# Kernel tuning notes

Measured on AMD Instinct MI355X. Metric: run time of the kernel, lower is better.

## Reference

```python
import jax, jax.numpy as jnp
import numpy as np
import math

NUM_HEADS = 3
WINDOW = 7


def _shift_masks(ws):
    # row_mask: block mask for windows wrapping across the bottom edge
    half = ws * (ws // 2)  # 21 for ws=7
    row = np.zeros((ws * ws, ws * ws), np.float32)
    row[-half:, :-half] = -np.inf
    row[:-half, -half:] = -np.inf
    # column_mask = rearrange(row, '(r w1) (c w2) -> (w1 r) (w2 c)')
    col = row.reshape(ws, ws, ws, ws).transpose(1, 0, 3, 2).reshape(ws * ws, ws * ws)
    return jnp.asarray(row), jnp.asarray(col)


def setup_inputs() -> dict:
    key = jax.random.key(0)
    ks = jax.random.split(key, 5)
    B, S, E = 64, 3136, 96
    return {
        'x': jax.random.normal(ks[0], (B, S, E), jnp.float32),
        'w1': jax.random.normal(ks[1], (3 * E, E), jnp.float32) * 0.05,
        'b1': jax.random.normal(ks[2], (3 * E,), jnp.float32) * 0.05,
        'w2': jax.random.normal(ks[3], (E, E), jnp.float32) * 0.05,
        'b2': jax.random.normal(ks[4], (E,), jnp.float32) * 0.05,
    }


def reference(x, w1, b1, w2, b2):
    b, S, E = x.shape
    h = w = int(math.sqrt(S))          # 56
    ws = WINDOW
    H = NUM_HEADS
    Eh = E // H                        # head dim = 32
    nh, nw = h // ws, w // ws          # windows per axis = 8
    scale = 1.0 / math.sqrt(E / H)
    # faithful to original: forward shift = -ws//2 = -4, inverse shift = ws//2 = 3
    shift_fwd = -ws // 2
    shift_bwd = ws // 2

    qkv = x @ w1.T + b1                              # [b, S, 3E]
    qkv = qkv.reshape(b, h, w, E, 3)                 # (c K) split, K fastest
    qkv = jnp.roll(qkv, (shift_fwd, shift_fwd), axis=(1, 2))
    # b (nh m1) (nw m2) (H Eh) K -> b H nh nw (m1 m2) Eh K
    qkv = qkv.reshape(b, nh, ws, nw, ws, H, Eh, 3)
    qkv = qkv.transpose(0, 5, 1, 3, 2, 4, 6, 7).reshape(b, H, nh, nw, ws * ws, Eh, 3)
    Q, K, V = qkv[..., 0], qkv[..., 1], qkv[..., 2]

    s = jnp.einsum('bHhwme,bHhwne->bHhwmn', Q, K) * scale  # [b,H,nh,nw,49,49]
    row_mask, col_mask = _shift_masks(ws)
    s = s.at[:, :, -1, :].add(row_mask)   # last row of windows
    s = s.at[:, :, :, -1].add(col_mask)   # last column of windows

    att = jax.nn.softmax(s, axis=-1)
    o = jnp.einsum('bHhwmn,bHhwne->bHhwme', att, V)        # [b,H,nh,nw,49,Eh]
    # b H nh nw (m1 m2) Eh -> b (nh m1) (nw m2) (H Eh)
    o = o.reshape(b, H, nh, nw, ws, ws, Eh)
    o = o.transpose(0, 2, 4, 3, 5, 1, 6).reshape(b, h, w, E)
    o = jnp.roll(o, (shift_bwd, shift_bwd), axis=(1, 2))
    o = o.reshape(b, S, E)
    return o @ w2.T + b2
```

## Files before the change

kernel.cpp:

```cpp
#include <hip/hip_runtime.h>


typedef _Float16 f16;
typedef _Float16 f16x4 __attribute__((ext_vector_type(4)));
typedef _Float16 f16x8 __attribute__((ext_vector_type(8)));
typedef float f32x4 __attribute__((ext_vector_type(4)));

static __device__ __forceinline__ f32x4 mfma16(f16x8 a, f16x8 b, f32x4 c) {
    return __builtin_amdgcn_mfma_f32_16x16x32_f16(a, b, c, 0, 0, 0);
}
static __device__ __forceinline__ f16x8 cvt8(const float* __restrict__ p) {
    float4 f0 = *(const float4*)(p);
    float4 f1 = *(const float4*)(p + 4);
    f16x8 h;
    h[0]=(f16)f0.x; h[1]=(f16)f0.y; h[2]=(f16)f0.z; h[3]=(f16)f0.w;
    h[4]=(f16)f1.x; h[5]=(f16)f1.y; h[6]=(f16)f1.z; h[7]=(f16)f1.w;
    return h;
}

#define SMEM_BYTES 38208
#define OFF_Q  7056
#define OFF_K  17248
#define OFF_VT 27440

template<bool WS>
__global__ __launch_bounds__(256, 4) void swin_fused(
    const float* __restrict__ x, const float* __restrict__ w1,
    const float* __restrict__ b1, const float* __restrict__ w2,
    const float* __restrict__ b2, float* __restrict__ out,
    const f16* __restrict__ w1p, const f16* __restrict__ w2p,
    const float* __restrict__ b1p)
{
    __shared__ __align__(16) char smem[SMEM_BYTES];
    f16* p_s  = (f16*)(smem);
    f16* q_s  = (f16*)(smem + OFF_Q);
    f16* k_s  = (f16*)(smem + OFF_K);
    f16* vt_s = (f16*)(smem + OFF_VT);
    f16* o_s  = q_s;

    const int tid  = threadIdx.x;
    const int wv   = tid >> 6;
    const int lane = tid & 63;
    const int lrow = lane & 15;
    const int lq   = lane >> 4;

    const int bx = blockIdx.x;
    const int b  = bx >> 6;
    const int wz = bx & 63;
    const int wh = wz >> 3;
    const int ww = wz & 7;

    const float* xb = x + b * (3136 * 96);

    if (tid < 96) {
        #pragma unroll
        for (int p7 = 49; p7 < 56; ++p7) vt_s[tid * 56 + p7] = (f16)0.f;
    }
    if (tid < 8) vt_s[96 * 56 + tid] = (f16)0.f;

    {
        f16x8 bf[5][3];
        float bias[5];
        int   kq[5], cm[5];
        #pragma unroll
        for (int t = 0; t < 5; ++t) {
            int nt = wv + 4 * t;
            if (nt < 18) {
                int col = nt * 16 + lrow;
                int kqv = nt / 6;
                int c96 = col - kqv * 96;
                if constexpr (WS) {
                    #pragma unroll
                    for (int ks = 0; ks < 3; ++ks)
                        bf[t][ks] = *(const f16x8*)(w1p + col * 96 + ks * 32 + lq * 8);
                    bias[t] = b1p[col];
                } else {
                    int srow = c96 * 3 + kqv;
                    #pragma unroll
                    for (int ks = 0; ks < 3; ++ks)
                        bf[t][ks] = cvt8(w1 + srow * 96 + ks * 32 + lq * 8);
                    bias[t] = b1[srow];
                }
                kq[t] = kqv; cm[t] = c96;
            } else { kq[t] = -1; cm[t] = 0; bias[t] = 0.f; }
        }
        #pragma unroll
        for (int mt = 0; mt < 4; ++mt) {
            int p  = mt * 16 + lrow; if (p > 48) p = 48;
            int i  = p / 7, j = p - i * 7;
            int r  = wh * 7 + i + 4; if (r >= 56) r -= 56;
            int c  = ww * 7 + j + 4; if (c >= 56) c -= 56;
            const float* xr = xb + (r * 56 + c) * 96;
            f16x8 af[3];
            #pragma unroll
            for (int ks = 0; ks < 3; ++ks) af[ks] = cvt8(xr + ks * 32 + lq * 8);
            int rbase = mt * 16 + lq * 4;
            #pragma unroll
            for (int t = 0; t < 5; ++t) {
                if (kq[t] < 0) continue;
                f32x4 acc = {0.f, 0.f, 0.f, 0.f};
                #pragma unroll
                for (int ks = 0; ks < 3; ++ks) acc = mfma16(af[ks], bf[t][ks], acc);
                if (kq[t] == 0) {
                    #pragma unroll
                    for (int r2 = 0; r2 < 4; ++r2) {
                        int row = rbase + r2;
                        if (row < 49) q_s[row * 104 + cm[t]] = (f16)(acc[r2] + bias[t]);
                    }
                } else if (kq[t] == 1) {
                    #pragma unroll
                    for (int r2 = 0; r2 < 4; ++r2) {
                        int row = rbase + r2;
                        if (row < 49) k_s[row * 104 + cm[t]] = (f16)(acc[r2] + bias[t]);
                    }
                } else {
                    f16x4 pk;
                    #pragma unroll
                    for (int r2 = 0; r2 < 4; ++r2) pk[r2] = (f16)(acc[r2] + bias[t]);
                    if (rbase < 45)      *(f16x4*)(vt_s + cm[t] * 56 + rbase) = pk;
                    else if (rbase == 48) vt_s[cm[t] * 56 + 48] = pk[0];
                }
            }
        }
    }
    __syncthreads();

    const bool mrow = (wh == 7), mcol = (ww == 7);
    const float scale = 0.17677669529663687f;
    const int mt = wv;
    const int arow  = mt * 16 + lrow;
    const int mbase = mt * 16 + lq * 4;

    #pragma unroll
    for (int hh = 0; hh < 3; ++hh) {
        f16x8 aq = *(const f16x8*)(q_s + arow * 104 + hh * 32 + lq * 8);
        f32x4 sc[4];
        #pragma unroll
        for (int nt = 0; nt < 4; ++nt) {
            f16x8 bk = *(const f16x8*)(k_s + (nt * 16 + lrow) * 104 + hh * 32 + lq * 8);
            f32x4 z = {0.f, 0.f, 0.f, 0.f};
            sc[nt] = mfma16(aq, bk, z);
        }
        float ev[4][4], vmax[4], esum[4];
        #pragma unroll
        for (int r2 = 0; r2 < 4; ++r2) vmax[r2] = -3e38f;
        #pragma unroll
        for (int nt = 0; nt < 4; ++nt) {
            int  nn  = nt * 16 + lrow;
            bool nok = nn < 49;
            bool nge = nn >= 28, n4 = (nn % 7) >= 4;
            #pragma unroll
            for (int r2 = 0; r2 < 4; ++r2) {
                int  mm = mbase + r2;
                bool ok = nok && (!mrow || ((mm >= 28) == nge))
                              && (!mcol || (((mm % 7) >= 4) == n4));
                float v = ok ? sc[nt][r2] * scale : -3e38f;
                ev[nt][r2] = v;
                vmax[r2] = fmaxf(vmax[r2], v);
            }
        }
        #pragma unroll
        for (int r2 = 0; r2 < 4; ++r2) {
            float m0 = vmax[r2];
            m0 = fmaxf(m0, __shfl_xor(m0, 1));
            m0 = fmaxf(m0, __shfl_xor(m0, 2));
            m0 = fmaxf(m0, __shfl_xor(m0, 4));
            m0 = fmaxf(m0, __shfl_xor(m0, 8));
            vmax[r2] = m0;
            esum[r2] = 0.f;
        }
        #pragma unroll
        for (int nt = 0; nt < 4; ++nt)
            #pragma unroll
            for (int r2 = 0; r2 < 4; ++r2) {
                float e = (ev[nt][r2] > -1e38f) ? __expf(ev[nt][r2] - vmax[r2]) : 0.f;
                ev[nt][r2] = e;
                esum[r2] += e;
            }
        #pragma unroll
        for (int r2 = 0; r2 < 4; ++r2) {
            float s = esum[r2];
            s += __shfl_xor(s, 1);
            s += __shfl_xor(s, 2);
            s += __shfl_xor(s, 4);
            s += __shfl_xor(s, 8);
            esum[r2] = 1.0f / s;
        }
        #pragma unroll
        for (int nt = 0; nt < 4; ++nt)
            #pragma unroll
            for (int r2 = 0; r2 < 4; ++r2) {
                int mm = mbase + r2;
                if (mm < 49)
                    p_s[mm * 72 + nt * 16 + lrow] = (f16)(ev[nt][r2] * esum[r2]);
            }

        f16x8 ap0 = *(const f16x8*)(p_s + arow * 72 + lq * 8);
        f16x8 ap1 = *(const f16x8*)(p_s + arow * 72 + 32 + lq * 8);
        #pragma unroll
        for (int et = 0; et < 2; ++et) {
            int vrow = hh * 32 + et * 16 + lrow;
            f16x8 bv0 = *(const f16x8*)(vt_s + vrow * 56 + lq * 8);
            f16x8 bv1 = *(const f16x8*)(vt_s + vrow * 56 + 32 + lq * 8);
            f32x4 z = {0.f, 0.f, 0.f, 0.f};
            f32x4 acc = mfma16(ap0, bv0, z);
            acc = mfma16(ap1, bv1, acc);
            #pragma unroll
            for (int r2 = 0; r2 < 4; ++r2) {
                int row = mbase + r2;
                if (row < 49)
                    o_s[row * 104 + hh * 32 + et * 16 + lrow] = (f16)acc[r2];
            }
        }
    }

    {
        f16x8 ao[3];
        #pragma unroll
        for (int ks = 0; ks < 3; ++ks)
            ao[ks] = *(const f16x8*)(o_s + arow * 104 + ks * 32 + lq * 8);
        int opos[4];
        #pragma unroll
        for (int r2 = 0; r2 < 4; ++r2) {
            int m  = mbase + r2;
            int mm = (m < 49) ? m : 48;
            int i  = mm / 7, j = mm - i * 7;
            int orow = wh * 7 + i + 3; if (orow >= 56) orow -= 56;
            int ocol = ww * 7 + j + 3; if (ocol >= 56) ocol -= 56;
            opos[r2] = (b * 3136 + orow * 56 + ocol) * 96;
        }
        #pragma unroll
        for (int nt = 0; nt < 6; ++nt) {
            int eo = nt * 16 + lrow;
            f32x4 acc = {0.f, 0.f, 0.f, 0.f};
            #pragma unroll
            for (int ks = 0; ks < 3; ++ks) {
                f16x8 hb;
                if constexpr (WS)
                    hb = *(const f16x8*)(w2p + eo * 96 + ks * 32 + lq * 8);
                else
                    hb = cvt8(w2 + eo * 96 + ks * 32 + lq * 8);
                acc = mfma16(ao[ks], hb, acc);
            }
            float bias = b2[eo];
            #pragma unroll
            for (int r2 = 0; r2 < 4; ++r2)
                if (mbase + r2 < 49) out[opos[r2] + eo] = acc[r2] + bias;
        }
    }
}

__global__ void prep_weights(const float* __restrict__ w1, const float* __restrict__ b1,
                             const float* __restrict__ w2,
                             f16* __restrict__ w1p, f16* __restrict__ w2p,
                             float* __restrict__ b1p)
{
    int idx = blockIdx.x * 256 + threadIdx.x;
    if (idx < 27648) {
        int np = idx / 96, k = idx - np * 96;
        int kq = np / 96, c96 = np - kq * 96;
        w1p[idx] = (f16)w1[(c96 * 3 + kq) * 96 + k];
    } else if (idx < 36864) {
        int i2 = idx - 27648;
        w2p[i2] = (f16)w2[i2];
    } else if (idx < 37152) {
        int np = idx - 36864;
        int kq = np / 96, c96 = np - kq * 96;
        b1p[np] = b1[c96 * 3 + kq];
    }
}

extern "C" void kernel_launch(void* const* d_in, const int* in_sizes, int n_in,
                              void* d_out, int out_size, void* d_ws, size_t ws_size,
                              hipStream_t stream) {
    const float* x  = (const float*)d_in[0];
    const float* w1 = (const float*)d_in[1];
    const float* b1 = (const float*)d_in[2];
    const float* w2 = (const float*)d_in[3];
    const float* b2 = (const float*)d_in[4];
    float* out = (float*)d_out;

    const size_t need = 27648u * 2 + 9216u * 2 + 288u * 4;
    if (ws_size >= need) {
        f16*   w1p = (f16*)d_ws;
        f16*   w2p = w1p + 27648;
        float* b1p = (float*)(w2p + 9216);
        prep_weights<<<dim3(146), dim3(256), 0, stream>>>(w1, b1, w2, w1p, w2p, b1p);
        swin_fused<true><<<dim3(4096), dim3(256), 0, stream>>>(
            x, w1, b1, w2, b2, out, w1p, w2p, b1p);
    } else {
        swin_fused<false><<<dim3(4096), dim3(256), 0, stream>>>(
            x, w1, b1, w2, b2, out, nullptr, nullptr, nullptr);
    }
}
```

Before: 226.5 us.

## Transpose MFMA operands so softmax stays in registers and stores vectorize

Swaps the A/B operands of the QKV, score, PV and output-projection MFMAs, so each lane owns one query row and the column results land contiguous per lane. The softmax reductions are then mostly in-register with two cross-lane shuffles, normalization is deferred to the PV output, and P is redistributed with register shuffles instead of being written to and read back from a shared-memory P buffer. This frees shared memory, allowing launch bounds to rise to 5 blocks per CU, and turns the Q/K, O and final output stores into 4-wide vector writes. The cost is extra shuffle instructions and more register pressure under the tighter occupancy bound.

New measurement: 258.9 us. 1.14x slower.

```diff
diff --git a/kernel.cpp b/kernel.cpp
--- a/kernel.cpp
+++ b/kernel.cpp
@@ -2,6 +2,7 @@
 
 
 typedef _Float16 f16;
+typedef _Float16 f16x2 __attribute__((ext_vector_type(2)));
 typedef _Float16 f16x4 __attribute__((ext_vector_type(4)));
 typedef _Float16 f16x8 __attribute__((ext_vector_type(8)));
 typedef float f32x4 __attribute__((ext_vector_type(4)));
@@ -18,13 +19,15 @@
     return h;
 }
 
-#define SMEM_BYTES 38208
-#define OFF_Q  7056
-#define OFF_K  17248
-#define OFF_VT 27440
+#define SMEM_BYTES 31152
+#define OFF_K  10192
+#define OFF_VT 20384
+
+union U2 { int i; f16x2 h; };
+union U8 { int i[4]; f16x8 h; };
 
 template<bool WS>
-__global__ __launch_bounds__(256, 4) void swin_fused(
+__global__ __launch_bounds__(256, 5) void swin_fused(
     const float* __restrict__ x, const float* __restrict__ w1,
     const float* __restrict__ b1, const float* __restrict__ w2,
     const float* __restrict__ b2, float* __restrict__ out,
@@ -32,8 +35,7 @@
     const float* __restrict__ b1p)
 {
     __shared__ __align__(16) char smem[SMEM_BYTES];
-    f16* p_s  = (f16*)(smem);
-    f16* q_s  = (f16*)(smem + OFF_Q);
+    f16* q_s  = (f16*)(smem);
     f16* k_s  = (f16*)(smem + OFF_K);
     f16* vt_s = (f16*)(smem + OFF_VT);
     f16* o_s  = q_s;
@@ -60,65 +62,74 @@
 
     {
         f16x8 bf[5][3];
-        float bias[5];
-        int   kq[5], cm[5];
+        int   kq[5], cb[5];
         #pragma unroll
         for (int t = 0; t < 5; ++t) {
-            int nt = wv + 4 * t;
-            if (nt < 18) {
-                int col = nt * 16 + lrow;
-                int kqv = nt / 6;
-                int c96 = col - kqv * 96;
+            int ot = wv + 4 * t;
+            if (ot < 18) {
+                int kqv = ot / 6;
+                kq[t] = kqv;
+                cb[t] = (ot - kqv * 6) * 16;
                 if constexpr (WS) {
                     #pragma unroll
                     for (int ks = 0; ks < 3; ++ks)
-                        bf[t][ks] = *(const f16x8*)(w1p + col * 96 + ks * 32 + lq * 8);
-                    bias[t] = b1p[col];
+                        bf[t][ks] = *(const f16x8*)(w1p + (ot*16 + lrow)*96 + ks*32 + lq*8);
                 } else {
-                    int srow = c96 * 3 + kqv;
+                    int srowA = (ot*16 + lrow - kqv*96) * 3 + kqv;
                     #pragma unroll
                     for (int ks = 0; ks < 3; ++ks)
-                        bf[t][ks] = cvt8(w1 + srow * 96 + ks * 32 + lq * 8);
-                    bias[t] = b1[srow];
+                        bf[t][ks] = cvt8(w1 + srowA*96 + ks*32 + lq*8);
                 }
-                kq[t] = kqv; cm[t] = c96;
-            } else { kq[t] = -1; cm[t] = 0; bias[t] = 0.f; }
-        }
-        #pragma unroll
-        for (int mt = 0; mt < 4; ++mt) {
-            int p  = mt * 16 + lrow; if (p > 48) p = 48;
-            int i  = p / 7, j = p - i * 7;
+            } else kq[t] = -1;
+        }
+        #pragma unroll
+        for (int pt = 0; pt < 4; ++pt) {
+            int p  = pt * 16 + lrow;
+            int pc = (p < 49) ? p : 48;
+            int i  = pc / 7, j = pc - i * 7;
             int r  = wh * 7 + i + 4; if (r >= 56) r -= 56;
             int c  = ww * 7 + j + 4; if (c >= 56) c -= 56;
             const float* xr = xb + (r * 56 + c) * 96;
-            f16x8 af[3];
-            #pragma unroll
-            for (int ks = 0; ks < 3; ++ks) af[ks] = cvt8(xr + ks * 32 + lq * 8);
-            int rbase = mt * 16 + lq * 4;
+            f16x8 xf[3];
+            #pragma unroll
+            for (int ks = 0; ks < 3; ++ks) xf[ks] = cvt8(xr + ks * 32 + lq * 8);
+            const bool pok = (p < 49);
             #pragma unroll
             for (int t = 0; t < 5; ++t) {
                 if (kq[t] < 0) continue;
+                int ot = wv + 4 * t;
                 f32x4 acc = {0.f, 0.f, 0.f, 0.f};
-                #pragma unroll
-                for (int ks = 0; ks < 3; ++ks) acc = mfma16(af[ks], bf[t][ks], acc);
-                if (kq[t] == 0) {
-                    #pragma unroll
-                    for (int r2 = 0; r2 < 4; ++r2) {
-                        int row = rbase + r2;
-                        if (row < 49) q_s[row * 104 + cm[t]] = (f16)(acc[r2] + bias[t]);
+                if (kq[t] == 2) {
+                    #pragma unroll
+                    for (int ks = 0; ks < 3; ++ks) acc = mfma16(xf[ks], bf[t][ks], acc);
+                    float bc;
+                    if constexpr (WS) bc = b1p[ot*16 + lrow];
+                    else              bc = b1[(ot*16 + lrow - 192)*3 + 2];
+                    int cc = cb[t] + lrow;
+                    f16x4 pk;
+                    #pragma unroll
+                    for (int i2 = 0; i2 < 4; ++i2) pk[i2] = (f16)(acc[i2] + bc);
+                    int p4 = pt * 16 + lq * 4;
+                    if (p4 < 45)       *(f16x4*)(vt_s + cc * 56 + p4) = pk;
+                    else if (p4 == 48) vt_s[cc * 56 + 48] = pk[0];
+                } else {
+                    #pragma unroll
+                    for (int ks = 0; ks < 3; ++ks) acc = mfma16(bf[t][ks], xf[ks], acc);
+                    if (pok) {
+                        f32x4 br;
+                        if constexpr (WS) {
+                            br = *(const f32x4*)(b1p + ot*16 + lq*4);
+                        } else {
+                            #pragma unroll
+                            for (int i2 = 0; i2 < 4; ++i2)
+                                br[i2] = b1[(ot*16 + lq*4 + i2 - kq[t]*96)*3 + kq[t]];
+                        }
+                        f16x4 pk;
+                        #pragma unroll
+                        for (int i2 = 0; i2 < 4; ++i2) pk[i2] = (f16)(acc[i2] + br[i2]);
+                        f16* dst = (kq[t] == 0 ? q_s : k_s) + p * 104 + cb[t] + lq * 4;
+                        *(f16x4*)dst = pk;
                     }
-                } else if (kq[t] == 1) {
-                    #pragma unroll
-                    for (int r2 = 0; r2 < 4; ++r2) {
-                        int row = rbase + r2;
-                        if (row < 49) k_s[row * 104 + cm[t]] = (f16)(acc[r2] + bias[t]);
-                    }
-                } else {
-                    f16x4 pk;
-                    #pragma unroll
-                    for (int r2 = 0; r2 < 4; ++r2) pk[r2] = (f16)(acc[r2] + bias[t]);
-                    if (rbase < 45)      *(f16x4*)(vt_s + cm[t] * 56 + rbase) = pk;
-                    else if (rbase == 48) vt_s[cm[t] * 56 + 48] = pk[0];
                 }
             }
         }
@@ -127,125 +138,134 @@
 
     const bool mrow = (wh == 7), mcol = (ww == 7);
     const float scale = 0.17677669529663687f;
-    const int mt = wv;
-    const int arow  = mt * 16 + lrow;
-    const int mbase = mt * 16 + lq * 4;
+    const int m = wv * 16 + lrow;
+
+    float mv[16];
+    {
+        const bool am = (m >= 28);
+        const bool a4 = (m % 7) >= 4;
+        #pragma unroll
+        for (int nt = 0; nt < 4; ++nt)
+            #pragma unroll
+            for (int i2 = 0; i2 < 4; ++i2) {
+                int nn = nt * 16 + lq * 4 + i2;
+                bool ok = (nn < 49)
+                       && (!mrow || (am == (nn >= 28)))
+                       && (!mcol || (a4 == ((nn % 7) >= 4)));
+                mv[nt*4 + i2] = ok ? 0.f : -3e38f;
+            }
+    }
+    const int idxA = lrow + 32 * (lq & 1);
+    const int idxB = idxA + 16;
+
+    f16x8 bq[3];
+    #pragma unroll
+    for (int hh = 0; hh < 3; ++hh)
+        bq[hh] = *(const f16x8*)(q_s + m * 104 + hh * 32 + lq * 8);
 
     #pragma unroll
     for (int hh = 0; hh < 3; ++hh) {
-        f16x8 aq = *(const f16x8*)(q_s + arow * 104 + hh * 32 + lq * 8);
         f32x4 sc[4];
         #pragma unroll
         for (int nt = 0; nt < 4; ++nt) {
-            f16x8 bk = *(const f16x8*)(k_s + (nt * 16 + lrow) * 104 + hh * 32 + lq * 8);
+            f16x8 ak = *(const f16x8*)(k_s + (nt*16 + lrow)*104 + hh*32 + lq*8);
             f32x4 z = {0.f, 0.f, 0.f, 0.f};
-            sc[nt] = mfma16(aq, bk, z);
-        }
-        float ev[4][4], vmax[4], esum[4];
-        #pragma unroll
-        for (int r2 = 0; r2 < 4; ++r2) vmax[r2] = -3e38f;
-        #pragma unroll
-        for (int nt = 0; nt < 4; ++nt) {
-            int  nn  = nt * 16 + lrow;
-            bool nok = nn < 49;
-            bool nge = nn >= 28, n4 = (nn % 7) >= 4;
-            #pragma unroll
-            for (int r2 = 0; r2 < 4; ++r2) {
-                int  mm = mbase + r2;
-                bool ok = nok && (!mrow || ((mm >= 28) == nge))
-                              && (!mcol || (((mm % 7) >= 4) == n4));
-                float v = ok ? sc[nt][r2] * scale : -3e38f;
-                ev[nt][r2] = v;
-                vmax[r2] = fmaxf(vmax[r2], v);
-            }
-        }
-        #pragma unroll
-        for (int r2 = 0; r2 < 4; ++r2) {
-            float m0 = vmax[r2];
-            m0 = fmaxf(m0, __shfl_xor(m0, 1));
-            m0 = fmaxf(m0, __shfl_xor(m0, 2));
-            m0 = fmaxf(m0, __shfl_xor(m0, 4));
-            m0 = fmaxf(m0, __shfl_xor(m0, 8));
-            vmax[r2] = m0;
-            esum[r2] = 0.f;
-        }
-        #pragma unroll
-        for (int nt = 0; nt < 4; ++nt)
-            #pragma unroll
-            for (int r2 = 0; r2 < 4; ++r2) {
-                float e = (ev[nt][r2] > -1e38f) ? __expf(ev[nt][r2] - vmax[r2]) : 0.f;
-                ev[nt][r2] = e;
-                esum[r2] += e;
-            }
-        #pragma unroll
-        for (int r2 = 0; r2 < 4; ++r2) {
-            float s = esum[r2];
-            s += __shfl_xor(s, 1);
-            s += __shfl_xor(s, 2);
-            s += __shfl_xor(s, 4);
-            s += __shfl_xor(s, 8);
-            esum[r2] = 1.0f / s;
-        }
-        #pragma unroll
-        for (int nt = 0; nt < 4; ++nt)
-            #pragma unroll
-            for (int r2 = 0; r2 < 4; ++r2) {
-                int mm = mbase + r2;
-                if (mm < 49)
-                    p_s[mm * 72 + nt * 16 + lrow] = (f16)(ev[nt][r2] * esum[r2]);
-            }
-
-        f16x8 ap0 = *(const f16x8*)(p_s + arow * 72 + lq * 8);
-        f16x8 ap1 = *(const f16x8*)(p_s + arow * 72 + 32 + lq * 8);
+            sc[nt] = mfma16(ak, bq[hh], z);
+        }
+        f16x8 va[2][2];
         #pragma unroll
         for (int et = 0; et < 2; ++et) {
             int vrow = hh * 32 + et * 16 + lrow;
-            f16x8 bv0 = *(const f16x8*)(vt_s + vrow * 56 + lq * 8);
-            f16x8 bv1 = *(const f16x8*)(vt_s + vrow * 56 + 32 + lq * 8);
+            va[et][0] = *(const f16x8*)(vt_s + vrow * 56 + lq * 8);
+            va[et][1] = *(const f16x8*)(vt_s + vrow * 56 + 32 + lq * 8);
+        }
+        float ev[16];
+        #pragma unroll
+        for (int nt = 0; nt < 4; ++nt)
+            #pragma unroll
+            for (int i2 = 0; i2 < 4; ++i2)
+                ev[nt*4 + i2] = fmaf(sc[nt][i2], scale, mv[nt*4 + i2]);
+        float tm[8];
+        #pragma unroll
+        for (int k2 = 0; k2 < 8; ++k2) tm[k2] = fmaxf(ev[2*k2], ev[2*k2+1]);
+        #pragma unroll
+        for (int k2 = 0; k2 < 4; ++k2) tm[k2] = fmaxf(tm[k2], tm[k2+4]);
+        float vm = fmaxf(fmaxf(tm[0], tm[1]), fmaxf(tm[2], tm[3]));
+        vm = fmaxf(vm, __shfl_xor(vm, 16));
+        vm = fmaxf(vm, __shfl_xor(vm, 32));
+        #pragma unroll
+        for (int k2 = 0; k2 < 16; ++k2) ev[k2] = __expf(ev[k2] - vm);
+        float ts[8];
+        #pragma unroll
+        for (int k2 = 0; k2 < 8; ++k2) ts[k2] = ev[2*k2] + ev[2*k2+1];
+        #pragma unroll
+        for (int k2 = 0; k2 < 4; ++k2) ts[k2] += ts[k2+4];
+        float s = (ts[0] + ts[1]) + (ts[2] + ts[3]);
+        s += __shfl_xor(s, 16);
+        s += __shfl_xor(s, 32);
+        float inv = 1.0f / s;
+
+        int pd[4][2];
+        #pragma unroll
+        for (int nt = 0; nt < 4; ++nt) {
+            U2 u0, u1;
+            u0.h[0] = (f16)ev[nt*4+0]; u0.h[1] = (f16)ev[nt*4+1];
+            u1.h[0] = (f16)ev[nt*4+2]; u1.h[1] = (f16)ev[nt*4+3];
+            pd[nt][0] = u0.i; pd[nt][1] = u1.i;
+        }
+        U8 ub0, ub1;
+        #pragma unroll
+        for (int w = 0; w < 4; ++w) {
+            int idx = (w < 2) ? idxA : idxB;
+            int rr  = w & 1;
+            int a0v = __shfl(pd[0][rr], idx);
+            int a1v = __shfl(pd[1][rr], idx);
+            ub0.i[w] = (lq & 2) ? a1v : a0v;
+            int c0v = __shfl(pd[2][rr], idx);
+            int c1v = __shfl(pd[3][rr], idx);
+            ub1.i[w] = (lq & 2) ? c1v : c0v;
+        }
+        #pragma unroll
+        for (int et = 0; et < 2; ++et) {
             f32x4 z = {0.f, 0.f, 0.f, 0.f};
-            f32x4 acc = mfma16(ap0, bv0, z);
-            acc = mfma16(ap1, bv1, acc);
-            #pragma unroll
-            for (int r2 = 0; r2 < 4; ++r2) {
-                int row = mbase + r2;
-                if (row < 49)
-                    o_s[row * 104 + hh * 32 + et * 16 + lrow] = (f16)acc[r2];
+            f32x4 oc = mfma16(va[et][0], ub0.h, z);
+            oc = mfma16(va[et][1], ub1.h, oc);
+            if (m < 49) {
+                f16x4 pk;
+                #pragma unroll
+                for (int i2 = 0; i2 < 4; ++i2) pk[i2] = (f16)(oc[i2] * inv);
+                *(f16x4*)(o_s + m * 104 + hh * 32 + et * 16 + lq * 4) = pk;
             }
         }
     }
 
     {
-        f16x8 ao[3];
+        f16x8 bo[3];
         #pragma unroll
         for (int ks = 0; ks < 3; ++ks)
-            ao[ks] = *(const f16x8*)(o_s + arow * 104 + ks * 32 + lq * 8);
-        int opos[4];
-        #pragma unroll
-        for (int r2 = 0; r2 < 4; ++r2) {
-            int m  = mbase + r2;
-            int mm = (m < 49) ? m : 48;
-            int i  = mm / 7, j = mm - i * 7;
-            int orow = wh * 7 + i + 3; if (orow >= 56) orow -= 56;
-            int ocol = ww * 7 + j + 3; if (ocol >= 56) ocol -= 56;
-            opos[r2] = (b * 3136 + orow * 56 + ocol) * 96;
-        }
-        #pragma unroll
-        for (int nt = 0; nt < 6; ++nt) {
-            int eo = nt * 16 + lrow;
+            bo[ks] = *(const f16x8*)(o_s + m * 104 + ks * 32 + lq * 8);
+        int mm2 = (m < 49) ? m : 48;
+        int i = mm2 / 7, j = mm2 - i * 7;
+        int orow = wh * 7 + i + 3; if (orow >= 56) orow -= 56;
+        int ocol = ww * 7 + j + 3; if (ocol >= 56) ocol -= 56;
+        float* op = out + (size_t)(b * 3136 + orow * 56 + ocol) * 96;
+        #pragma unroll
+        for (int ot2 = 0; ot2 < 6; ++ot2) {
             f32x4 acc = {0.f, 0.f, 0.f, 0.f};
             #pragma unroll
             for (int ks = 0; ks < 3; ++ks) {
-                f16x8 hb;
+                f16x8 aw;
                 if constexpr (WS)
-                    hb = *(const f16x8*)(w2p + eo * 96 + ks * 32 + lq * 8);
+                    aw = *(const f16x8*)(w2p + (ot2*16 + lrow)*96 + ks*32 + lq*8);
                 else
-                    hb = cvt8(w2 + eo * 96 + ks * 32 + lq * 8);
-                acc = mfma16(ao[ks], hb, acc);
-            }
-            float bias = b2[eo];
-            #pragma unroll
-            for (int r2 = 0; r2 < 4; ++r2)
-                if (mbase + r2 < 49) out[opos[r2] + eo] = acc[r2] + bias;
+                    aw = cvt8(w2 + (ot2*16 + lrow)*96 + ks*32 + lq*8);
+                acc = mfma16(aw, bo[ks], acc);
+            }
+            f32x4 bias = *(const f32x4*)(b2 + ot2 * 16 + lq * 4);
+            if (m < 49) {
+                f32x4 o4 = acc + bias;
+                *(f32x4*)(op + ot2 * 16 + lq * 4) = o4;
+            }
         }
     }
 }
```
